# Kernel optimization log

Measured on AMD Instinct MI355X. Metric: run time of the kernel, lower is better.

The kernel has to match this reference:

```python
import jax, jax.numpy as jnp
import numpy as np

B, S, E, H, D = 2, 2048, 1024, 16, 64  # batch, seq(=max_seq_len), embed_dim, heads, atten_dim


def setup_inputs() -> dict:
    key = jax.random.key(0)
    ks = jax.random.split(key, 9)
    s = 0.02
    return {
        "x": jax.random.normal(ks[0], (B, S, E), jnp.float32),
        "Wq": jax.random.normal(ks[1], (H, E, D), jnp.float32) * s,
        "Wk": jax.random.normal(ks[2], (H, E, D), jnp.float32) * s,
        "Wv": jax.random.normal(ks[3], (H, E, D), jnp.float32) * s,
        "bq": jax.random.normal(ks[4], (H, D), jnp.float32) * s,
        "bk": jax.random.normal(ks[5], (H, D), jnp.float32) * s,
        "bv": jax.random.normal(ks[6], (H, D), jnp.float32) * s,
        "Wp": jax.random.normal(ks[7], (H * D, E), jnp.float32) * s,
        "bp": jax.random.normal(ks[8], (E,), jnp.float32) * s,
    }


def reference(x, Wq, Wk, Wv, bq, bk, bv, Wp, bp):
    scale = jnp.sqrt(jnp.float32(D))
    # per-head projections, all heads at once: [B,H,S,D]
    q = jnp.einsum("bse,hed->bhsd", x, Wq) + bq[:, None, :]
    k = jnp.einsum("bse,hed->bhsd", x, Wk) + bk[:, None, :]
    v = jnp.einsum("bse,hed->bhsd", x, Wv) + bv[:, None, :]
    # causal scores [B,H,S,S], additive -inf mask above diagonal (as in the buffer)
    score = jnp.einsum("bhsd,bhtd->bhst", q, k) / scale
    mask = jnp.triu(jnp.full((S, S), -jnp.inf, jnp.float32), k=1)
    score = score + mask
    probs = jax.nn.softmax(score, axis=-1)
    attn = jnp.einsum("bhst,bhtd->bhsd", probs, v)
    # concat heads -> [B,S,H*D], then projection + ReLU
    concat = attn.transpose(0, 2, 1, 3).reshape(B, S, H * D)
    out = jax.nn.relu(concat @ Wp + bp)
    return out
```

## Files before the change

kernel.cpp:

```cpp
#include <hip/hip_runtime.h>

#define S_LEN 2048
#define E_DIM 1024
#define H_NUM 16
#define D_DIM 64

typedef unsigned short u16;
using bf16x8 = __attribute__((ext_vector_type(8))) short;
using f32x4  = __attribute__((ext_vector_type(4))) float;

#define MFMA16(A, B, C) __builtin_amdgcn_mfma_f32_16x16x32_bf16(A, B, C, 0, 0, 0)
#define QSCALE 0.18033688011112042f

__device__ __forceinline__ u16 f2bf(float f) {
    unsigned u = __float_as_uint(f);
    u += 0x7fffu + ((u >> 16) & 1u);
    return (u16)(u >> 16);
}
__device__ __forceinline__ f32x4 fzero4() { f32x4 z; z[0]=0.f; z[1]=0.f; z[2]=0.f; z[3]=0.f; return z; }

__device__ __forceinline__ unsigned cvtpk(float a, float b) {
    unsigned r;
    asm("v_cvt_pk_bf16_f32 %0, %1, %2" : "=v"(r) : "v"(a), "v"(b));
    return r;
}
__device__ __forceinline__ float fexp2(float x) {
#if __has_builtin(__builtin_amdgcn_exp2f)
    return __builtin_amdgcn_exp2f(x);
#else
    float r; asm("v_exp_f32 %0, %1" : "=v"(r) : "v"(x)); return r;
#endif
}
__device__ __forceinline__ float frcp(float x) {
#if __has_builtin(__builtin_amdgcn_rcpf)
    return __builtin_amdgcn_rcpf(x);
#else
    float r; asm("v_rcp_f32 %0, %1" : "=v"(r) : "v"(x)); return r;
#endif
}

__device__ __forceinline__ void gll16(const u16* g, u16* l) {
    __builtin_amdgcn_global_load_lds(
        (const __attribute__((address_space(1))) void*)g,
        (__attribute__((address_space(3))) void*)l, 16, 0, 0);
}

__device__ __forceinline__ void stage64(const u16* __restrict__ g, int gstride,
                                        u16* l, int wave, int lane) {
    #pragma unroll
    for (int i = 0; i < 2; i++) {
        const int r  = wave * 16 + i * 8 + (lane >> 3);
        const int sl = (lane & 7) ^ (r & 7);
        gll16(g + (size_t)r * gstride + sl * 8, l + (wave * 16 + i * 8) * 64);
    }
}
__device__ __forceinline__ bf16x8 ldswz(const u16* t, int rr, int hh, int quad) {
    const int sl = ((hh << 2) + quad) ^ (rr & 7);
    return *(const bf16x8*)(t + rr * 64 + sl * 8);
}

__global__ __launch_bounds__(256) void cvt_bf16(const float* __restrict__ in, u16* __restrict__ outp, int n) {
    int i4 = (blockIdx.x * 256 + threadIdx.x) * 4;
    if (i4 < n) {
        float4 f = *(const float4*)(in + i4);
        unsigned lo = (unsigned)f2bf(f.x) | ((unsigned)f2bf(f.y) << 16);
        unsigned hi = (unsigned)f2bf(f.z) | ((unsigned)f2bf(f.w) << 16);
        uint2 p; p.x = lo; p.y = hi;
        *(uint2*)(outp + i4) = p;
    }
}

__device__ __forceinline__ void cvt_t_tile(const float* __restrict__ bin, u16* __restrict__ bout,
                                           int R, int C, int r0, int c0) {
    __shared__ float t[64][65];
    const int tid = threadIdx.x;
    const int lr = tid >> 2, lc = (tid & 3) * 16;

    const float* src = bin + (size_t)(r0 + lr) * C + c0 + lc;
    #pragma unroll
    for (int j = 0; j < 4; j++) {
        float4 f = *(const float4*)(src + j * 4);
        t[lr][lc + j * 4 + 0] = f.x; t[lr][lc + j * 4 + 1] = f.y;
        t[lr][lc + j * 4 + 2] = f.z; t[lr][lc + j * 4 + 3] = f.w;
    }
    __syncthreads();

    u16* dst = bout + (size_t)(c0 + lr) * R + r0 + lc;
    u16 vals[16];
    #pragma unroll
    for (int i = 0; i < 16; i++) vals[i] = f2bf(t[lc + i][lr]);
    uint4 pa, pb;
    pa.x = vals[0] | (vals[1] << 16);  pa.y = vals[2] | (vals[3] << 16);
    pa.z = vals[4] | (vals[5] << 16);  pa.w = vals[6] | (vals[7] << 16);
    pb.x = vals[8] | (vals[9] << 16);  pb.y = vals[10] | (vals[11] << 16);
    pb.z = vals[12] | (vals[13] << 16); pb.w = vals[14] | (vals[15] << 16);
    *(uint4*)dst = pa;
    *(uint4*)(dst + 8) = pb;
}

__global__ __launch_bounds__(256) void cvt_bf16_t(const float* __restrict__ in, u16* __restrict__ outp,
                                                  int R, int C) {
    const float* bin = in + (size_t)blockIdx.z * R * C;
    u16* bout = outp + (size_t)blockIdx.z * R * C;
    cvt_t_tile(bin, bout, R, C, blockIdx.y * 64, blockIdx.x * 64);
}

__global__ __launch_bounds__(256) void cvt_w3_t(
    const float* __restrict__ Wq, const float* __restrict__ Wk, const float* __restrict__ Wv,
    u16* __restrict__ wqt, u16* __restrict__ wkt, u16* __restrict__ wvt) {
    const int which = blockIdx.z >> 4, bh = blockIdx.z & 15;
    const float* in = (which == 0) ? Wq : (which == 1) ? Wk : Wv;
    u16* outp = (which == 0) ? wqt : (which == 1) ? wkt : wvt;
    const float* bin = in + (size_t)bh * E_DIM * D_DIM;
    u16* bout = outp + (size_t)bh * E_DIM * D_DIM;
    cvt_t_tile(bin, bout, E_DIM, D_DIM, blockIdx.y * 64, 0);
}

__global__ __launch_bounds__(256) void qkv_gemm(
    const u16* __restrict__ xb, const u16* __restrict__ wcat,
    const float* __restrict__ bq, const float* __restrict__ bk, const float* __restrict__ bv,
    u16* __restrict__ oq, u16* __restrict__ okk, u16* __restrict__ ov)
{
    const int m0 = blockIdx.x * 128;
    const int n0 = blockIdx.y * 128;

    __shared__ u16 As[128 * 32];
    __shared__ u16 Bs[128 * 32];

    const int tid  = threadIdx.x;
    const int wave = tid >> 6, lane = tid & 63, quad = lane >> 4, l16 = lane & 15;
    const int mh = wave >> 1, nh = wave & 1;

    const int lrow = lane >> 2, lcol = (lane & 3) * 8;
    const u16* aBase = xb   + (size_t)(m0 + wave * 32 + lrow) * E_DIM + lcol;
    const u16* bBase = wcat + (size_t)(n0 + wave * 32 + lrow) * E_DIM + lcol;
    u16* aLds0 = &As[(wave * 32     ) * 32];
    u16* aLds1 = &As[(wave * 32 + 16) * 32];
    u16* bLds0 = &Bs[(wave * 32     ) * 32];
    u16* bLds1 = &Bs[(wave * 32 + 16) * 32];

    f32x4 acc[4][4];
    #pragma unroll
    for (int j = 0; j < 4; j++)
        #pragma unroll
        for (int mi = 0; mi < 4; mi++) acc[j][mi] = fzero4();

    for (int k0 = 0; k0 < E_DIM; k0 += 32) {
        __syncthreads();
        gll16(aBase + k0,                 aLds0);
        gll16(aBase + k0 + 16 * E_DIM,    aLds1);
        gll16(bBase + k0,                 bLds0);
        gll16(bBase + k0 + 16 * E_DIM,    bLds1);
        __syncthreads();

        bf16x8 af[4];
        #pragma unroll
        for (int mi = 0; mi < 4; mi++)
            af[mi] = *(const bf16x8*)(&As[(mh * 64 + mi * 16 + l16) * 32 + quad * 8]);
        #pragma unroll
        for (int j = 0; j < 4; j++) {
            bf16x8 bfv = *(const bf16x8*)(&Bs[(nh * 64 + j * 16 + l16) * 32 + quad * 8]);
            #pragma unroll
            for (int mi = 0; mi < 4; mi++)
                acc[j][mi] = MFMA16(af[mi], bfv, acc[j][mi]);
        }
    }

    const int t = n0 >> 10;
    if (t < 2) {
        const float scl = (t == 0) ? QSCALE : 1.0f;
        const float* bias = (t == 0) ? bq : bk;
        u16* dst = (t == 0) ? oq : okk;
        #pragma unroll
        for (int j = 0; j < 4; j++) {
            const int n = n0 + nh * 64 + j * 16 + l16;
            const int h = (n >> 6) & 15, d = n & 63;
            float bia = bias[h * D_DIM + d];
            #pragma unroll
            for (int mi = 0; mi < 4; mi++) {
                #pragma unroll
                for (int r = 0; r < 4; r++) {
                    int m = m0 + mh * 64 + mi * 16 + quad * 4 + r;
                    int b = m >> 11, s = m & 2047;
                    dst[((size_t)(b * H_NUM + h) * S_LEN + s) * D_DIM + d] =
                        f2bf((acc[j][mi][r] + bia) * scl);
                }
            }
        }
    } else {
        #pragma unroll
        for (int j = 0; j < 4; j++) {
            const int n = n0 + nh * 64 + j * 16 + l16;
            const int h = (n >> 6) & 15, d = n & 63;
            float bia = bv[h * D_DIM + d];
            #pragma unroll
            for (int mi = 0; mi < 4; mi++) {
                int m = m0 + mh * 64 + mi * 16 + quad * 4;
                int b = m >> 11, s = m & 2047;
                uint2 pk;
                pk.x = cvtpk(acc[j][mi][0] + bia, acc[j][mi][1] + bia);
                pk.y = cvtpk(acc[j][mi][2] + bia, acc[j][mi][3] + bia);
                *(uint2*)(&ov[((size_t)(b * H_NUM + h) * D_DIM + d) * S_LEN + s]) = pk;
            }
        }
    }
}

__global__ __launch_bounds__(256) void attn_fwd(
    const u16* __restrict__ q, const u16* __restrict__ k, const u16* __restrict__ vt,
    u16* __restrict__ concat)
{
    const int p  = blockIdx.x;
    const int qa = p, qb = 31 - p;
    const int h  = blockIdx.y;
    const int bb = blockIdx.z;

    const size_t headoff = (size_t)(bb * H_NUM + h) * S_LEN * D_DIM;
    const u16* qh  = q  + headoff;
    const u16* kh  = k  + headoff;
    const u16* vth = vt + headoff;

    __shared__ u16 QaL[64 * 64];
    __shared__ u16 QbL[64 * 64];
    __shared__ u16 Ks[2][64 * 64];
    __shared__ u16 Vts[2][64 * 64];
    __shared__ u16 Ps[4][16 * 72];

    const int tid  = threadIdx.x;
    const int wave = tid >> 6, lane = tid & 63, quad = lane >> 4, l16 = lane & 15;

    stage64(qh + (size_t)qa * 64 * D_DIM, D_DIM, QaL,    wave, lane);
    stage64(qh + (size_t)qb * 64 * D_DIM, D_DIM, QbL,    wave, lane);
    stage64(kh,                           D_DIM, Ks[0],  wave, lane);
    stage64(vth,                          S_LEN, Vts[0], wave, lane);
    __syncthreads();

    bf16x8 bqa0 = ldswz(QaL, wave * 16 + l16, 0, quad);
    bf16x8 bqa1 = ldswz(QaL, wave * 16 + l16, 1, quad);
    bf16x8 bqb0 = ldswz(QbL, wave * 16 + l16, 0, quad);
    bf16x8 bqb1 = ldswz(QbL, wave * 16 + l16, 1, quad);

    f32x4 oa[4], ob[4];
    #pragma unroll
    for (int nt = 0; nt < 4; nt++) { oa[nt] = fzero4(); ob[nt] = fzero4(); }
    float la = 0.f, lb = 0.f;

    const int qga = qa * 64 + wave * 16 + l16;
    const int qgb = qb * 64 + wave * 16 + l16;

    for (int kt = 0; kt <= qb; kt++) {
        if (kt) __syncthreads();
        if (kt < qb) {
            stage64(kh + (size_t)(kt + 1) * 64 * D_DIM, D_DIM, Ks[(kt + 1) & 1],  wave, lane);
            stage64(vth + (kt + 1) * 64,                S_LEN, Vts[(kt + 1) & 1], wave, lane);
        }
        const u16* Kc = Ks[kt & 1];
        const u16* Vc = Vts[kt & 1];
        const bool both = (kt <= qa);

        f32x4 stb[4], sta[4];
        #pragma unroll
        for (int nt = 0; nt < 4; nt++) {
            const int rr = nt * 16 + l16;
            bf16x8 ak0 = ldswz(Kc, rr, 0, quad);
            bf16x8 ak1 = ldswz(Kc, rr, 1, quad);
            stb[nt] = MFMA16(ak0, bqb0, fzero4());
            stb[nt] = MFMA16(ak1, bqb1, stb[nt]);
            if (both) {
                sta[nt] = MFMA16(ak0, bqa0, fzero4());
                sta[nt] = MFMA16(ak1, bqa1, sta[nt]);
            }
        }

        bf16x8 bv0[4], bv1[4];

        {
            u16* pw = &Ps[wave][0];
            #pragma unroll
            for (int nt = 0; nt < 4; nt++) {
                float pe[4];
                if (kt == qb) {
                    #pragma unroll
                    for (int r = 0; r < 4; r++) {
                        int kkg = kt * 64 + nt * 16 + quad * 4 + r;
                        pe[r] = (kkg > qgb) ? 0.f : fexp2(stb[nt][r]);
                    }
                } else {
                    #pragma unroll
                    for (int r = 0; r < 4; r++) pe[r] = fexp2(stb[nt][r]);
                }
                lb += (pe[0] + pe[1]) + (pe[2] + pe[3]);
                uint2 pk;
                pk.x = cvtpk(pe[0], pe[1]);
                pk.y = cvtpk(pe[2], pe[3]);
                *(uint2*)(&pw[l16 * 72 + nt * 16 + quad * 4]) = pk;
            }
            bf16x8 ap0 = *(const bf16x8*)(&Ps[wave][l16 * 72 + quad * 8]);
            bf16x8 ap1 = *(const bf16x8*)(&Ps[wave][l16 * 72 + 32 + quad * 8]);
            #pragma unroll
            for (int nt = 0; nt < 4; nt++) {
                bv0[nt] = ldswz(Vc, nt * 16 + l16, 0, quad);
                bv1[nt] = ldswz(Vc, nt * 16 + l16, 1, quad);
                ob[nt] = MFMA16(ap0, bv0[nt], ob[nt]);
                ob[nt] = MFMA16(ap1, bv1[nt], ob[nt]);
            }
        }

        if (both) {
            u16* pw = &Ps[wave][0];
            #pragma unroll
            for (int nt = 0; nt < 4; nt++) {
                float pe[4];
                if (kt == qa) {
                    #pragma unroll
                    for (int r = 0; r < 4; r++) {
                        int kkg = kt * 64 + nt * 16 + quad * 4 + r;
                        pe[r] = (kkg > qga) ? 0.f : fexp2(sta[nt][r]);
                    }
                } else {
                    #pragma unroll
                    for (int r = 0; r < 4; r++) pe[r] = fexp2(sta[nt][r]);
                }
                la += (pe[0] + pe[1]) + (pe[2] + pe[3]);
                uint2 pk;
                pk.x = cvtpk(pe[0], pe[1]);
                pk.y = cvtpk(pe[2], pe[3]);
                *(uint2*)(&pw[l16 * 72 + nt * 16 + quad * 4]) = pk;
            }
            bf16x8 ap0 = *(const bf16x8*)(&Ps[wave][l16 * 72 + quad * 8]);
            bf16x8 ap1 = *(const bf16x8*)(&Ps[wave][l16 * 72 + 32 + quad * 8]);
            #pragma unroll
            for (int nt = 0; nt < 4; nt++) {
                oa[nt] = MFMA16(ap0, bv0[nt], oa[nt]);
                oa[nt] = MFMA16(ap1, bv1[nt], oa[nt]);
            }
        }
    }

    lb += __shfl_xor(lb, 16); lb += __shfl_xor(lb, 32);
    la += __shfl_xor(la, 16); la += __shfl_xor(la, 32);

    #pragma unroll
    for (int r = 0; r < 4; r++) {
        const int srcl = quad * 4 + r;
        float lbi = frcp(__shfl(lb, srcl));
        float lai = frcp(__shfl(la, srcl));
        int sqa = qa * 64 + wave * 16 + quad * 4 + r;
        int sqb = qb * 64 + wave * 16 + quad * 4 + r;
        #pragma unroll
        for (int nt = 0; nt < 4; nt++) {
            concat[((size_t)(bb * S_LEN + sqa)) * E_DIM + h * D_DIM + nt * 16 + l16] =
                f2bf(oa[nt][r] * lai);
            concat[((size_t)(bb * S_LEN + sqb)) * E_DIM + h * D_DIM + nt * 16 + l16] =
                f2bf(ob[nt][r] * lbi);
        }
    }
}

__global__ __launch_bounds__(256) void out_proj(
    const u16* __restrict__ concat, const u16* __restrict__ wpt,
    const float* __restrict__ bp, float* __restrict__ out)
{
    const int m0 = blockIdx.x * 128;
    const int n0 = blockIdx.y * 128;

    __shared__ u16 As[128 * 40];
    __shared__ u16 Bs[128 * 40];

    const int tid  = threadIdx.x;
    const int wave = tid >> 6, lane = tid & 63, quad = lane >> 4, l16 = lane & 15;
    const int mh = wave >> 1, nh = wave & 1;

    const int arow = tid >> 1, acol = (tid & 1) * 16;

    const u16* aptr = concat + (size_t)(m0 + arow) * E_DIM + acol;
    const u16* bptr = wpt + (size_t)(n0 + arow) * E_DIM + acol;

    f32x4 acc[4][4];
    #pragma unroll
    for (int j = 0; j < 4; j++)
        #pragma unroll
        for (int mi = 0; mi < 4; mi++) acc[j][mi] = fzero4();

    uint4 pA0, pA1, pB0, pB1;
    pA0 = *(const uint4*)(aptr);     pA1 = *(const uint4*)(aptr + 8);
    pB0 = *(const uint4*)(bptr);     pB1 = *(const uint4*)(bptr + 8);

    for (int k0 = 0; k0 < E_DIM; k0 += 32) {
        __syncthreads();
        *(uint4*)(&As[arow * 40 + acol    ]) = pA0;
        *(uint4*)(&As[arow * 40 + acol + 8]) = pA1;
        *(uint4*)(&Bs[arow * 40 + acol    ]) = pB0;
        *(uint4*)(&Bs[arow * 40 + acol + 8]) = pB1;
        __syncthreads();

        if (k0 + 32 < E_DIM) {
            pA0 = *(const uint4*)(aptr + k0 + 32);  pA1 = *(const uint4*)(aptr + k0 + 40);
            pB0 = *(const uint4*)(bptr + k0 + 32);  pB1 = *(const uint4*)(bptr + k0 + 40);
        }

        bf16x8 af[4];
        #pragma unroll
        for (int mi = 0; mi < 4; mi++)
            af[mi] = *(const bf16x8*)(&As[(mh * 64 + mi * 16 + l16) * 40 + quad * 8]);
        #pragma unroll
        for (int j = 0; j < 4; j++) {
            bf16x8 bfv = *(const bf16x8*)(&Bs[(nh * 64 + j * 16 + l16) * 40 + quad * 8]);
            #pragma unroll
            for (int mi = 0; mi < 4; mi++)
                acc[j][mi] = MFMA16(af[mi], bfv, acc[j][mi]);
        }
    }

    #pragma unroll
    for (int j = 0; j < 4; j++) {
        int n = n0 + nh * 64 + j * 16 + l16;
        float bia = bp[n];
        #pragma unroll
        for (int mi = 0; mi < 4; mi++) {
            #pragma unroll
            for (int r = 0; r < 4; r++) {
                int m = m0 + mh * 64 + mi * 16 + quad * 4 + r;
                out[(size_t)m * E_DIM + n] = fmaxf(acc[j][mi][r] + bia, 0.f);
            }
        }
    }
}

extern "C" void kernel_launch(void* const* d_in, const int* in_sizes, int n_in,
                              void* d_out, int out_size, void* d_ws, size_t ws_size,
                              hipStream_t stream)
{
    (void)in_sizes; (void)n_in; (void)out_size; (void)ws_size;
    const float* x  = (const float*)d_in[0];
    const float* Wq = (const float*)d_in[1];
    const float* Wk = (const float*)d_in[2];
    const float* Wv = (const float*)d_in[3];
    const float* bq = (const float*)d_in[4];
    const float* bk = (const float*)d_in[5];
    const float* bv = (const float*)d_in[6];
    const float* Wp = (const float*)d_in[7];
    const float* bp = (const float*)d_in[8];
    float* out = (float*)d_out;

    const size_t QKV_ELEMS = (size_t)2 * H_NUM * S_LEN * D_DIM;
    const size_t W_ELEMS   = (size_t)H_NUM * E_DIM * D_DIM;

    u16* q   = (u16*)d_ws;
    u16* k   = q   + QKV_ELEMS;
    u16* v   = k   + QKV_ELEMS;
    u16* cc  = v   + QKV_ELEMS;
    u16* xb  = cc  + QKV_ELEMS;
    u16* wqt = xb  + QKV_ELEMS;
    u16* wkt = wqt + W_ELEMS;
    u16* wvt = wkt + W_ELEMS;
    u16* wpt = wvt + W_ELEMS;

    cvt_bf16<<<dim3(4096), 256, 0, stream>>>(x, xb, (int)QKV_ELEMS);
    cvt_w3_t<<<dim3(1, 16, 48), 256, 0, stream>>>(Wq, Wk, Wv, wqt, wkt, wvt);
    cvt_bf16_t<<<dim3(16, 16, 1), 256, 0, stream>>>(Wp, wpt, H_NUM * D_DIM, E_DIM);

    qkv_gemm<<<dim3(32, 24), 256, 0, stream>>>(xb, wqt, bq, bk, bv, q, k, v);
    attn_fwd<<<dim3(16, 16, 2), 256, 0, stream>>>(q, k, v, cc);
    out_proj<<<dim3(32, 8), 256, 0, stream>>>(cc, wpt, bp, out);
}
```

Baseline: 207.1 us.

## Widen QKV GEMM K-tile with swizzled LDS, coalesce V store, reorder attention

The QKV GEMM now stages a 64-wide K slice per iteration into XOR-swizzled LDS. This halves the barrier count and is meant to avoid bank conflicts. The V-output epilogue is transposed through LDS so each thread writes 16-byte coalesced rows instead of scattered 8-byte stores. The attention kernel uses a flattened 1D grid that interleaves the causal pair index, and adds launch_bounds occupancy 2. It also uses separate P buffers for the two query tiles so both exp phases finish before the PV MFMAs, with V loads hoisted earlier. Together these add extra syncs and LDS traffic in exchange.

New measurement: 191.7 us. 7.4% less time.

```diff
diff --git a/kernel.cpp b/kernel.cpp
--- a/kernel.cpp
+++ b/kernel.cpp
@@ -124,45 +124,46 @@
     const int m0 = blockIdx.x * 128;
     const int n0 = blockIdx.y * 128;
 
-    __shared__ u16 As[128 * 32];
-    __shared__ u16 Bs[128 * 32];
+    __shared__ u16 As[128 * 64];
+    __shared__ u16 Bs[128 * 64];
 
     const int tid  = threadIdx.x;
     const int wave = tid >> 6, lane = tid & 63, quad = lane >> 4, l16 = lane & 15;
     const int mh = wave >> 1, nh = wave & 1;
 
-    const int lrow = lane >> 2, lcol = (lane & 3) * 8;
-    const u16* aBase = xb   + (size_t)(m0 + wave * 32 + lrow) * E_DIM + lcol;
-    const u16* bBase = wcat + (size_t)(n0 + wave * 32 + lrow) * E_DIM + lcol;
-    u16* aLds0 = &As[(wave * 32     ) * 32];
-    u16* aLds1 = &As[(wave * 32 + 16) * 32];
-    u16* bLds0 = &Bs[(wave * 32     ) * 32];
-    u16* bLds1 = &Bs[(wave * 32 + 16) * 32];
-
     f32x4 acc[4][4];
     #pragma unroll
     for (int j = 0; j < 4; j++)
         #pragma unroll
         for (int mi = 0; mi < 4; mi++) acc[j][mi] = fzero4();
 
-    for (int k0 = 0; k0 < E_DIM; k0 += 32) {
+    for (int k0 = 0; k0 < E_DIM; k0 += 64) {
         __syncthreads();
-        gll16(aBase + k0,                 aLds0);
-        gll16(aBase + k0 + 16 * E_DIM,    aLds1);
-        gll16(bBase + k0,                 bLds0);
-        gll16(bBase + k0 + 16 * E_DIM,    bLds1);
+        #pragma unroll
+        for (int i = 0; i < 4; i++) {
+            const int r  = wave * 32 + i * 8 + (lane >> 3);
+            const int sl = (lane & 7) ^ (r & 7);
+            gll16(xb   + (size_t)(m0 + r) * E_DIM + k0 + sl * 8, &As[(wave * 32 + i * 8) * 64]);
+            gll16(wcat + (size_t)(n0 + r) * E_DIM + k0 + sl * 8, &Bs[(wave * 32 + i * 8) * 64]);
+        }
         __syncthreads();
 
-        bf16x8 af[4];
-        #pragma unroll
-        for (int mi = 0; mi < 4; mi++)
-            af[mi] = *(const bf16x8*)(&As[(mh * 64 + mi * 16 + l16) * 32 + quad * 8]);
-        #pragma unroll
-        for (int j = 0; j < 4; j++) {
-            bf16x8 bfv = *(const bf16x8*)(&Bs[(nh * 64 + j * 16 + l16) * 32 + quad * 8]);
-            #pragma unroll
-            for (int mi = 0; mi < 4; mi++)
-                acc[j][mi] = MFMA16(af[mi], bfv, acc[j][mi]);
+        #pragma unroll
+        for (int kq = 0; kq < 2; kq++) {
+            bf16x8 af[4];
+            #pragma unroll
+            for (int mi = 0; mi < 4; mi++) {
+                const int rr = mh * 64 + mi * 16 + l16;
+                af[mi] = *(const bf16x8*)(&As[rr * 64 + (((kq << 2) + quad) ^ (rr & 7)) * 8]);
+            }
+            #pragma unroll
+            for (int j = 0; j < 4; j++) {
+                const int rr = nh * 64 + j * 16 + l16;
+                bf16x8 bfv = *(const bf16x8*)(&Bs[rr * 64 + (((kq << 2) + quad) ^ (rr & 7)) * 8]);
+                #pragma unroll
+                for (int mi = 0; mi < 4; mi++)
+                    acc[j][mi] = MFMA16(af[mi], bfv, acc[j][mi]);
+            }
         }
     }
 
@@ -188,32 +189,57 @@
             }
         }
     } else {
-        #pragma unroll
-        for (int j = 0; j < 4; j++) {
-            const int n = n0 + nh * 64 + j * 16 + l16;
-            const int h = (n >> 6) & 15, d = n & 63;
-            float bia = bv[h * D_DIM + d];
-            #pragma unroll
-            for (int mi = 0; mi < 4; mi++) {
-                int m = m0 + mh * 64 + mi * 16 + quad * 4;
-                int b = m >> 11, s = m & 2047;
-                uint2 pk;
-                pk.x = cvtpk(acc[j][mi][0] + bia, acc[j][mi][1] + bia);
-                pk.y = cvtpk(acc[j][mi][2] + bia, acc[j][mi][3] + bia);
-                *(uint2*)(&ov[((size_t)(b * H_NUM + h) * D_DIM + d) * S_LEN + s]) = pk;
-            }
-        }
-    }
-}
-
-__global__ __launch_bounds__(256) void attn_fwd(
+        const int b  = m0 >> 11, s0 = m0 & 2047;
+        const int h0 = (n0 >> 6) & 15;
+        u16* Tb0 = As;
+        u16* Tb1 = Bs;
+        #pragma unroll
+        for (int pass = 0; pass < 2; ++pass) {
+            __syncthreads();
+            if (mh == pass) {
+                u16* Tb = nh ? Tb1 : Tb0;
+                #pragma unroll
+                for (int j = 0; j < 4; j++) {
+                    const int n = n0 + nh * 64 + j * 16 + l16;
+                    const int d = n & 63, hh = (n >> 6) & 15;
+                    const float bia = bv[hh * D_DIM + d];
+                    const int nl = j * 16 + l16;
+                    #pragma unroll
+                    for (int mi = 0; mi < 4; mi++) {
+                        uint2 pk;
+                        pk.x = cvtpk(acc[j][mi][0] + bia, acc[j][mi][1] + bia);
+                        pk.y = cvtpk(acc[j][mi][2] + bia, acc[j][mi][3] + bia);
+                        *(uint2*)(&Tb[nl * 72 + mi * 16 + quad * 4]) = pk;
+                    }
+                }
+            }
+            __syncthreads();
+            #pragma unroll
+            for (int g = 0; g < 4; ++g) {
+                const int rowi = g * 32 + (tid >> 3);
+                const int ml = (tid & 7) * 8;
+                const u16* srcp = (rowi < 64 ? Tb0 : Tb1) + (rowi & 63) * 72 + ml;
+                const int hh = h0 + (rowi >> 6), d = rowi & 63;
+                u16* dstp = ov + ((size_t)(b * H_NUM + hh) * D_DIM + d) * S_LEN
+                               + s0 + pass * 64 + ml;
+                *(uint4*)dstp = *(const uint4*)srcp;
+            }
+        }
+    }
+}
+
+__global__ __launch_bounds__(256, 2) void attn_fwd(
     const u16* __restrict__ q, const u16* __restrict__ k, const u16* __restrict__ vt,
     u16* __restrict__ concat)
 {
-    const int p  = blockIdx.x;
+    const int bid  = blockIdx.x;
+    const int halfg = bid >> 8;
+    const int pi   = (bid & 255) >> 5;
+    const int p    = halfg ? (15 - pi) : pi;
+    const int g    = bid & 31;
+    const int h    = g & 15;
+    const int bb   = g >> 4;
     const int qa = p, qb = 31 - p;
-    const int h  = blockIdx.y;
-    const int bb = blockIdx.z;
 
     const size_t headoff = (size_t)(bb * H_NUM + h) * S_LEN * D_DIM;
     const u16* qh  = q  + headoff;
@@ -224,7 +250,8 @@
     __shared__ u16 QbL[64 * 64];
     __shared__ u16 Ks[2][64 * 64];
     __shared__ u16 Vts[2][64 * 64];
-    __shared__ u16 Ps[4][16 * 72];
+    __shared__ u16 Psa[4][16 * 72];
+    __shared__ u16 Psb[4][16 * 72];
 
     const int tid  = threadIdx.x;
     const int wave = tid >> 6, lane = tid & 63, quad = lane >> 4, l16 = lane & 15;
@@ -248,8 +275,11 @@
     const int qga = qa * 64 + wave * 16 + l16;
     const int qgb = qb * 64 + wave * 16 + l16;
 
+    u16* pwa = &Psa[wave][0];
+    u16* pwb = &Psb[wave][0];
+
     for (int kt = 0; kt <= qb; kt++) {
-        if (kt) __syncthreads();
+        __syncthreads();
         if (kt < qb) {
             stage64(kh + (size_t)(kt + 1) * 64 * D_DIM, D_DIM, Ks[(kt + 1) & 1],  wave, lane);
             stage64(vth + (kt + 1) * 64,                S_LEN, Vts[(kt + 1) & 1], wave, lane);
@@ -273,41 +303,32 @@
         }
 
         bf16x8 bv0[4], bv1[4];
-
-        {
-            u16* pw = &Ps[wave][0];
-            #pragma unroll
-            for (int nt = 0; nt < 4; nt++) {
-                float pe[4];
-                if (kt == qb) {
-                    #pragma unroll
-                    for (int r = 0; r < 4; r++) {
-                        int kkg = kt * 64 + nt * 16 + quad * 4 + r;
-                        pe[r] = (kkg > qgb) ? 0.f : fexp2(stb[nt][r]);
-                    }
-                } else {
-                    #pragma unroll
-                    for (int r = 0; r < 4; r++) pe[r] = fexp2(stb[nt][r]);
+        #pragma unroll
+        for (int nt = 0; nt < 4; nt++) {
+            bv0[nt] = ldswz(Vc, nt * 16 + l16, 0, quad);
+            bv1[nt] = ldswz(Vc, nt * 16 + l16, 1, quad);
+        }
+
+        #pragma unroll
+        for (int nt = 0; nt < 4; nt++) {
+            float pe[4];
+            if (kt == qb) {
+                #pragma unroll
+                for (int r = 0; r < 4; r++) {
+                    int kkg = kt * 64 + nt * 16 + quad * 4 + r;
+                    pe[r] = (kkg > qgb) ? 0.f : fexp2(stb[nt][r]);
                 }
-                lb += (pe[0] + pe[1]) + (pe[2] + pe[3]);
-                uint2 pk;
-                pk.x = cvtpk(pe[0], pe[1]);
-                pk.y = cvtpk(pe[2], pe[3]);
-                *(uint2*)(&pw[l16 * 72 + nt * 16 + quad * 4]) = pk;
-            }
-            bf16x8 ap0 = *(const bf16x8*)(&Ps[wave][l16 * 72 + quad * 8]);
-            bf16x8 ap1 = *(const bf16x8*)(&Ps[wave][l16 * 72 + 32 + quad * 8]);
-            #pragma unroll
-            for (int nt = 0; nt < 4; nt++) {
-                bv0[nt] = ldswz(Vc, nt * 16 + l16, 0, quad);
-                bv1[nt] = ldswz(Vc, nt * 16 + l16, 1, quad);
-                ob[nt] = MFMA16(ap0, bv0[nt], ob[nt]);
-                ob[nt] = MFMA16(ap1, bv1[nt], ob[nt]);
-            }
-        }
-
+            } else {
+                #pragma unroll
+                for (int r = 0; r < 4; r++) pe[r] = fexp2(stb[nt][r]);
+            }
+            lb += (pe[0] + pe[1]) + (pe[2] + pe[3]);
+            uint2 pk;
+            pk.x = cvtpk(pe[0], pe[1]);
+            pk.y = cvtpk(pe[2], pe[3]);
+            *(uint2*)(&pwb[l16 * 72 + nt * 16 + quad * 4]) = pk;
+        }
         if (both) {
-            u16* pw = &Ps[wave][0];
             #pragma unroll
             for (int nt = 0; nt < 4; nt++) {
                 float pe[4];
@@ -325,10 +346,22 @@
                 uint2 pk;
                 pk.x = cvtpk(pe[0], pe[1]);
                 pk.y = cvtpk(pe[2], pe[3]);
-                *(uint2*)(&pw[l16 * 72 + nt * 16 + quad * 4]) = pk;
-            }
-            bf16x8 ap0 = *(const bf16x8*)(&Ps[wave][l16 * 72 + quad * 8]);
-            bf16x8 ap1 = *(const bf16x8*)(&Ps[wave][l16 * 72 + 32 + quad * 8]);
+                *(uint2*)(&pwa[l16 * 72 + nt * 16 + quad * 4]) = pk;
+            }
+        }
+
+        {
+            bf16x8 ap0 = *(const bf16x8*)(&pwb[l16 * 72 + quad * 8]);
+            bf16x8 ap1 = *(const bf16x8*)(&pwb[l16 * 72 + 32 + quad * 8]);
+            #pragma unroll
+            for (int nt = 0; nt < 4; nt++) {
+                ob[nt] = MFMA16(ap0, bv0[nt], ob[nt]);
+                ob[nt] = MFMA16(ap1, bv1[nt], ob[nt]);
+            }
+        }
+        if (both) {
+            bf16x8 ap0 = *(const bf16x8*)(&pwa[l16 * 72 + quad * 8]);
+            bf16x8 ap1 = *(const bf16x8*)(&pwa[l16 * 72 + 32 + quad * 8]);
             #pragma unroll
             for (int nt = 0; nt < 4; nt++) {
                 oa[nt] = MFMA16(ap0, bv0[nt], oa[nt]);
@@ -461,6 +494,6 @@
     cvt_bf16_t<<<dim3(16, 16, 1), 256, 0, stream>>>(Wp, wpt, H_NUM * D_DIM, E_DIM);
 
     qkv_gemm<<<dim3(32, 24), 256, 0, stream>>>(xb, wqt, bq, bk, bv, q, k, v);
-    attn_fwd<<<dim3(16, 16, 2), 256, 0, stream>>>(q, k, v, cc);
+    attn_fwd<<<dim3(512), 256, 0, stream>>>(q, k, v, cc);
     out_proj<<<dim3(32, 8), 256, 0, stream>>>(cc, wpt, bp, out);
 }
```
